# Performance work log

Measured on AMD Instinct MI355X. Metric: run time of the kernel, lower is better.

Reference implementation:

```python
import jax, jax.numpy as jnp
import numpy as np

M, B, S, D, H = 8, 4, 512, 512, 8
HD = D // H  # head_dim = 64


def setup_inputs() -> dict:
    key = jax.random.key(0)
    k1, k2, k3 = jax.random.split(key, 3)
    x = jax.random.normal(k1, (M, B, S, D), dtype=jnp.float32)
    qkv_weight = jax.random.normal(k2, (M, D, 3 * D), dtype=jnp.float32) * 0.02
    proj_weight = jax.random.normal(k3, (M, D, D), dtype=jnp.float32) * 0.02
    return {"x": x, "qkv_weight": qkv_weight, "proj_weight": proj_weight}


def reference(x, qkv_weight, proj_weight):
    m, b, s, d = x.shape
    # model-axis batched QKV projection
    qkv = jnp.einsum('mbti,mio->mbto', x, qkv_weight)
    q, k, v = jnp.split(qkv, 3, axis=-1)
    # [m, b, h, s, hd]
    q = q.reshape(m, b, s, H, HD).transpose(0, 1, 3, 2, 4)
    k = k.reshape(m, b, s, H, HD).transpose(0, 1, 3, 2, 4)
    v = v.reshape(m, b, s, H, HD).transpose(0, 1, 3, 2, 4)
    att = jnp.einsum('mbhqd,mbhkd->mbhqk', q, k) / jnp.sqrt(jnp.float32(HD))
    causal = jnp.tril(jnp.ones((s, s), dtype=bool))
    att = jnp.where(causal, att, jnp.float32(-jnp.inf))
    att = jax.nn.softmax(att, axis=-1)
    y = jnp.einsum('mbhqk,mbhkd->mbhqd', att, v)
    y = y.transpose(0, 1, 3, 2, 4).reshape(m, b, s, d)
    return jnp.einsum('mbti,mio->mbto', y, proj_weight)
```

## Files before the change

### kernel.cpp

```cpp
#include <hip/hip_runtime.h>
#include <hip/hip_bf16.h>


typedef unsigned short u16;
typedef unsigned int u32;
typedef __attribute__((ext_vector_type(8))) short short8;
typedef __attribute__((ext_vector_type(4))) float f32x4;
typedef __attribute__((ext_vector_type(4))) unsigned short u16x4;
typedef __attribute__((ext_vector_type(8))) unsigned short u16x8;
typedef __attribute__((ext_vector_type(2))) unsigned int u32x2;

#define MFMA16(a, b, c) __builtin_amdgcn_mfma_f32_16x16x32_bf16((a), (b), (c), 0, 0, 0)

__device__ __forceinline__ u16 f2bf(float f) {
  union { __hip_bfloat16 h; u16 u; } cv;
  cv.h = __float2bfloat16(f);
  return cv.u;
}

__device__ __forceinline__ void gl_lds16(const u16* g, u16* l) {
  __builtin_amdgcn_global_load_lds(
      (const __attribute__((address_space(1))) void*)g,
      (__attribute__((address_space(3))) void*)l, 16, 0, 0);
}

__global__ __launch_bounds__(256) void xcast_kernel(const float* __restrict__ in,
                                                    u16* __restrict__ out, long n8) {
  long stride = (long)gridDim.x * 256;
  for (long i = blockIdx.x * 256L + threadIdx.x; i < n8; i += stride) {
    f32x4 a = *(const f32x4*)(in + i * 8);
    f32x4 b = *(const f32x4*)(in + i * 8 + 4);
    u16x8 o = {f2bf(a[0]), f2bf(a[1]), f2bf(a[2]), f2bf(a[3]),
               f2bf(b[0]), f2bf(b[1]), f2bf(b[2]), f2bf(b[3])};
    *(u16x8*)(out + i * 8) = o;
  }
}

__global__ __launch_bounds__(256) void wtrans_kernel(const float* __restrict__ in,
                                                     u16* __restrict__ out, int R, int C) {
  __shared__ float t[32][33];
  int m = blockIdx.z;
  const float* pin = in + (size_t)m * R * C;
  u16* pout = out + (size_t)m * R * C;
  int c0 = blockIdx.x * 32, r0 = blockIdx.y * 32;
  int tx = threadIdx.x, ty = threadIdx.y;
#pragma unroll
  for (int i = 0; i < 4; ++i) {
    int r = ty + i * 8;
    t[r][tx] = pin[(size_t)(r0 + r) * C + c0 + tx];
  }
  __syncthreads();
#pragma unroll
  for (int i = 0; i < 4; ++i) {
    int r = ty + i * 8;
    pout[(size_t)(c0 + r) * R + r0 + tx] = f2bf(t[tx][r]);
  }
}

__global__ __launch_bounds__(512) void qkv_gemm_kernel(const u16* __restrict__ XB,
                                                       const u16* __restrict__ WT,
                                                       u16* __restrict__ Q,
                                                       u16* __restrict__ K,
                                                       u16* __restrict__ VT) {
  __shared__ __attribute__((aligned(16))) u16 As[3][256 * 32];
  __shared__ __attribute__((aligned(16))) u16 Bs[3][128 * 32];
  int bid = blockIdx.x;
  int wgid = (bid & 7) * 96 + (bid >> 3);
  int m = wgid / 96;
  int rem = wgid % 96;
  int r0 = (rem / 12) * 256, c0 = (rem % 12) * 128;
  const u16* A = XB + (size_t)m * 2048 * 512;
  const u16* BT = WT + (size_t)m * 1536 * 512;
  int t = threadIdx.x;
  int lane = t & 63, w = t >> 6;
  int wr = (w >> 1) * 64, wc = (w & 1) * 64;
  int fr = lane & 15, fc = lane >> 4;

  int rA0 = t >> 2, sA0 = (t & 3) ^ ((rA0 >> 1) & 3);
  int rA1 = 128 + (t >> 2), sA1 = (t & 3) ^ ((rA1 >> 1) & 3);

  f32x4 acc[4][4];
#pragma unroll
  for (int i = 0; i < 4; ++i)
#pragma unroll
    for (int j = 0; j < 4; ++j) acc[i][j] = f32x4{0.f, 0.f, 0.f, 0.f};

#define QKV_STAGE(tile)                                                            \
  {                                                                                \
    int kk_ = (tile) * 32;                                                         \
    int b_ = (tile) % 3;                                                           \
    gl_lds16(A + (size_t)(r0 + rA0) * 512 + kk_ + sA0 * 8, &As[b_][w * 512]);      \
    gl_lds16(A + (size_t)(r0 + rA1) * 512 + kk_ + sA1 * 8, &As[b_][4096 + w * 512]); \
    gl_lds16(BT + (size_t)(c0 + rA0) * 512 + kk_ + sA0 * 8, &Bs[b_][w * 512]);     \
  }

#define QKV_COMPUTE(tile)                                                          \
  {                                                                                \
    int b_ = (tile) % 3;                                                           \
    short8 af[4], bf_[4];                                                          \
    _Pragma("unroll") for (int i = 0; i < 4; ++i) {                                \
      int row = wr + i * 16 + fr;                                                  \
      int sl = fc ^ ((row >> 1) & 3);                                              \
      af[i] = *(const short8*)&As[b_][row * 32 + sl * 8];                          \
    }                                                                              \
    _Pragma("unroll") for (int j = 0; j < 4; ++j) {                                \
      int row = wc + j * 16 + fr;                                                  \
      int sl = fc ^ ((row >> 1) & 3);                                              \
      bf_[j] = *(const short8*)&Bs[b_][row * 32 + sl * 8];                         \
    }                                                                              \
    _Pragma("unroll") for (int i = 0; i < 4; ++i)                                  \
      _Pragma("unroll") for (int j = 0; j < 4; ++j)                                \
        acc[i][j] = MFMA16(af[i], bf_[j], acc[i][j]);                              \
  }

  QKV_STAGE(0);
  QKV_STAGE(1);
  for (int ks = 0; ks < 14; ++ks) {
    asm volatile("s_waitcnt vmcnt(3)" ::: "memory");
    __builtin_amdgcn_sched_barrier(0);
    __builtin_amdgcn_s_barrier();
    QKV_STAGE(ks + 2);
    QKV_COMPUTE(ks);
    __builtin_amdgcn_sched_barrier(0);
  }
  asm volatile("s_waitcnt vmcnt(0)" ::: "memory");
  __builtin_amdgcn_sched_barrier(0);
  __builtin_amdgcn_s_barrier();
  QKV_COMPUTE(14);
  QKV_COMPUTE(15);

  int seg = c0 >> 9;
  if (seg == 2) {
#pragma unroll
    for (int i = 0; i < 4; ++i)
#pragma unroll
      for (int j = 0; j < 4; ++j) {
        int s0 = r0 + wr + i * 16 + fc * 4;
        int gcol = c0 + wc + j * 16 + fr;
        int cc = gcol & 511;
        int hh = cc >> 6, hd = cc & 63;
        int b = s0 >> 9, s = s0 & 511;
        size_t headoff = (size_t)((m * 4 + b) * 8 + hh) * 32768;
        u16x4 pk = {f2bf(acc[i][j][0]), f2bf(acc[i][j][1]),
                    f2bf(acc[i][j][2]), f2bf(acc[i][j][3])};
        *(u16x4*)(VT + headoff + (size_t)hd * 512 + s) = pk;
      }
  } else {
#pragma unroll
    for (int i = 0; i < 4; ++i)
#pragma unroll
      for (int j = 0; j < 4; ++j)
#pragma unroll
        for (int r = 0; r < 4; ++r) {
          int grow = r0 + wr + i * 16 + fc * 4 + r;
          int gcol = c0 + wc + j * 16 + fr;
          int b = grow >> 9, s = grow & 511;
          int cc = gcol & 511;
          int hh = cc >> 6, hd = cc & 63;
          size_t headoff = (size_t)((m * 4 + b) * 8 + hh) * 32768;
          u16 val = f2bf(acc[i][j][r]);
          if (seg == 0) Q[headoff + s * 64 + hd] = val;
          else          K[headoff + s * 64 + hd] = val;
        }
  }
}

__global__ __launch_bounds__(256) void attn_kernel(const u16* __restrict__ Qg,
                                                   const u16* __restrict__ Kg,
                                                   const u16* __restrict__ VTg,
                                                   u16* __restrict__ Yg) {
  __shared__ __attribute__((aligned(16))) u16 Ks[2][64 * 64];
  __shared__ __attribute__((aligned(16))) u16 Vs[2][64 * 64];
  __shared__ u16 Pl[4][16][72];
  int bid = blockIdx.x;
  int p = bid >> 8;
  int g = bid & 255;
  int h = g & 7, mb = g >> 3;
  int qtA = p, qtB = 7 - p;
  int t = threadIdx.x, lane = t & 63, w = t >> 6;
  int fr = lane & 15, fc = lane >> 4;
  size_t hoff = ((size_t)mb * 8 + h) * 32768;
  const u16* Q = Qg + hoff;
  const u16* K = Kg + hoff;
  const u16* V = VTg + hoff;
  const float SC = 0.125f * 1.44269504088896340736f;

  int qrowA = qtA * 64 + w * 16 + fr;
  int qrowB = qtB * 64 + w * 16 + fr;
  short8 qA0 = *(const short8*)(Q + (size_t)qrowA * 64 + fc * 8);
  short8 qA1 = *(const short8*)(Q + (size_t)qrowA * 64 + 32 + fc * 8);
  short8 qB0 = *(const short8*)(Q + (size_t)qrowB * 64 + fc * 8);
  short8 qB1 = *(const short8*)(Q + (size_t)qrowB * 64 + 32 + fc * 8);

  f32x4 accA[4], accB[4];
#pragma unroll
  for (int d = 0; d < 4; ++d) {
    accA[d] = f32x4{0.f, 0.f, 0.f, 0.f};
    accB[d] = f32x4{0.f, 0.f, 0.f, 0.f};
  }
  float mstA = -1e30f, lstA = 0.f, mstB = -1e30f, lstB = 0.f;

  int sr0 = t >> 3, ss0 = (t & 7) ^ (sr0 & 7);
  int sr1 = 32 + (t >> 3), ss1 = (t & 7) ^ (sr1 & 7);

#define ATTN_STAGE(kt_, buf_)                                                     \
  {                                                                               \
    int kb_ = (kt_) * 64;                                                         \
    gl_lds16(K + (size_t)(kb_ + sr0) * 64 + ss0 * 8, &Ks[buf_][w * 512]);         \
    gl_lds16(K + (size_t)(kb_ + sr1) * 64 + ss1 * 8, &Ks[buf_][2048 + w * 512]);  \
    gl_lds16(V + (size_t)sr0 * 512 + kb_ + ss0 * 8, &Vs[buf_][w * 512]);          \
    gl_lds16(V + (size_t)sr1 * 512 + kb_ + ss1 * 8, &Vs[buf_][2048 + w * 512]);   \
  }

  int qloc = w * 16 + fr;
  ATTN_STAGE(0, 0);

  for (int kt = 0; kt <= qtB; ++kt) {
    int cur = kt & 1;
    if (kt < qtB) {
      ATTN_STAGE(kt + 1, cur ^ 1);
      asm volatile("s_waitcnt vmcnt(4)" ::: "memory");
    } else {
      asm volatile("s_waitcnt vmcnt(0)" ::: "memory");
    }
    __builtin_amdgcn_sched_barrier(0);
    __builtin_amdgcn_s_barrier();

    auto tile_compute = [&](const short8& qf0, const short8& qf1, f32x4(&acc)[4],
                            float& mst, float& lst, bool diag) {
      f32x4 st[4];
#pragma unroll
      for (int sub = 0; sub < 4; ++sub) {
        int row = sub * 16 + fr;
        short8 kf0 = *(const short8*)&Ks[cur][row * 64 + ((fc ^ (row & 7)) & 7) * 8];
        short8 kf1 = *(const short8*)&Ks[cur][row * 64 + (((4 + fc) ^ (row & 7)) & 7) * 8];
        f32x4 z = f32x4{0.f, 0.f, 0.f, 0.f};
        z = MFMA16(kf0, qf0, z);
        st[sub] = MFMA16(kf1, qf1, z);
      }
      float pv[4][4];
      float mt = -3e30f;
#pragma unroll
      for (int sub = 0; sub < 4; ++sub)
#pragma unroll
        for (int r = 0; r < 4; ++r) {
          float v = st[sub][r] * SC;
          if (diag && (sub * 16 + fc * 4 + r) > qloc) v = -1e30f;
          pv[sub][r] = v;
          mt = fmaxf(mt, v);
        }
      mt = fmaxf(mt, __shfl_xor(mt, 16));
      mt = fmaxf(mt, __shfl_xor(mt, 32));
      float mn = fmaxf(mst, mt);
      float al = __builtin_amdgcn_exp2f(mst - mn);
      mst = mn;
      float rs = 0.f;
#pragma unroll
      for (int sub = 0; sub < 4; ++sub)
#pragma unroll
        for (int r = 0; r < 4; ++r) {
          float e = __builtin_amdgcn_exp2f(pv[sub][r] - mn);
          pv[sub][r] = e;
          rs += e;
        }
      rs += __shfl_xor(rs, 16);
      rs += __shfl_xor(rs, 32);
      lst = lst * al + rs;
#pragma unroll
      for (int d = 0; d < 4; ++d) acc[d] *= al;

#pragma unroll
      for (int sub = 0; sub < 4; ++sub) {
        u32 lo = (u32)f2bf(pv[sub][0]) | ((u32)f2bf(pv[sub][1]) << 16);
        u32 hi = (u32)f2bf(pv[sub][2]) | ((u32)f2bf(pv[sub][3]) << 16);
        *(u32x2*)&Pl[w][fr][sub * 16 + fc * 4] = u32x2{lo, hi};
      }
#pragma unroll
      for (int dt = 0; dt < 4; ++dt)
#pragma unroll
        for (int kc = 0; kc < 2; ++kc) {
          int row = dt * 16 + fr;
          short8 vf = *(const short8*)&Vs[cur][row * 64 + (((kc * 4 + fc) ^ (row & 7)) & 7) * 8];
          short8 pb = *(const short8*)&Pl[w][fr][kc * 32 + fc * 8];
          acc[dt] = MFMA16(vf, pb, acc[dt]);
        }
    };

    if (kt <= qtA) tile_compute(qA0, qA1, accA, mstA, lstA, kt == qtA);
    tile_compute(qB0, qB1, accB, mstB, lstB, kt == qtB);

    asm volatile("s_waitcnt lgkmcnt(0)" ::: "memory");
    __builtin_amdgcn_sched_barrier(0);
    __builtin_amdgcn_s_barrier();
  }

  float invA = 1.0f / lstA, invB = 1.0f / lstB;
#pragma unroll
  for (int dt = 0; dt < 4; ++dt) {
    u16x4 oA = {f2bf(accA[dt][0] * invA), f2bf(accA[dt][1] * invA),
                f2bf(accA[dt][2] * invA), f2bf(accA[dt][3] * invA)};
    *(u16x4*)(Yg + ((size_t)mb * 512 + qrowA) * 512 + h * 64 + dt * 16 + fc * 4) = oA;
    u16x4 oB = {f2bf(accB[dt][0] * invB), f2bf(accB[dt][1] * invB),
                f2bf(accB[dt][2] * invB), f2bf(accB[dt][3] * invB)};
    *(u16x4*)(Yg + ((size_t)mb * 512 + qrowB) * 512 + h * 64 + dt * 16 + fc * 4) = oB;
  }
}

__global__ __launch_bounds__(512) void proj_gemm_kernel(const u16* __restrict__ Y,
                                                        const u16* __restrict__ PT,
                                                        float* __restrict__ OUT) {
  __shared__ __attribute__((aligned(16))) u16 As[3][256 * 32];
  __shared__ __attribute__((aligned(16))) u16 Bs[3][128 * 32];
  int bid = blockIdx.x;
  int wgid = (bid & 7) * 32 + (bid >> 3);
  int m = wgid / 32;
  int rem = wgid % 32;
  int r0 = (rem / 4) * 256, c0 = (rem % 4) * 128;
  const u16* A = Y + (size_t)m * 2048 * 512;
  const u16* BT = PT + (size_t)m * 512 * 512;
  float* C = OUT + (size_t)m * 2048 * 512;
  int t = threadIdx.x;
  int lane = t & 63, w = t >> 6;
  int wr = (w >> 1) * 64, wc = (w & 1) * 64;
  int fr = lane & 15, fc = lane >> 4;

  int rA0 = t >> 2, sA0 = (t & 3) ^ ((rA0 >> 1) & 3);
  int rA1 = 128 + (t >> 2), sA1 = (t & 3) ^ ((rA1 >> 1) & 3);

  f32x4 acc[4][4];
#pragma unroll
  for (int i = 0; i < 4; ++i)
#pragma unroll
    for (int j = 0; j < 4; ++j) acc[i][j] = f32x4{0.f, 0.f, 0.f, 0.f};

#define PROJ_STAGE(tile)                                                           \
  {                                                                                \
    int kk_ = (tile) * 32;                                                         \
    int b_ = (tile) % 3;                                                           \
    gl_lds16(A + (size_t)(r0 + rA0) * 512 + kk_ + sA0 * 8, &As[b_][w * 512]);      \
    gl_lds16(A + (size_t)(r0 + rA1) * 512 + kk_ + sA1 * 8, &As[b_][4096 + w * 512]); \
    gl_lds16(BT + (size_t)(c0 + rA0) * 512 + kk_ + sA0 * 8, &Bs[b_][w * 512]);     \
  }

#define PROJ_COMPUTE(tile)                                                         \
  {                                                                                \
    int b_ = (tile) % 3;                                                           \
    short8 af[4], bf_[4];                                                          \
    _Pragma("unroll") for (int i = 0; i < 4; ++i) {                                \
      int row = wr + i * 16 + fr;                                                  \
      int sl = fc ^ ((row >> 1) & 3);                                              \
      af[i] = *(const short8*)&As[b_][row * 32 + sl * 8];                          \
    }                                                                              \
    _Pragma("unroll") for (int j = 0; j < 4; ++j) {                                \
      int row = wc + j * 16 + fr;                                                  \
      int sl = fc ^ ((row >> 1) & 3);                                              \
      bf_[j] = *(const short8*)&Bs[b_][row * 32 + sl * 8];                         \
    }                                                                              \
    _Pragma("unroll") for (int i = 0; i < 4; ++i)                                  \
      _Pragma("unroll") for (int j = 0; j < 4; ++j)                                \
        acc[i][j] = MFMA16(af[i], bf_[j], acc[i][j]);                              \
  }

  PROJ_STAGE(0);
  PROJ_STAGE(1);
  for (int ks = 0; ks < 14; ++ks) {
    asm volatile("s_waitcnt vmcnt(3)" ::: "memory");
    __builtin_amdgcn_sched_barrier(0);
    __builtin_amdgcn_s_barrier();
    PROJ_STAGE(ks + 2);
    PROJ_COMPUTE(ks);
    __builtin_amdgcn_sched_barrier(0);
  }
  asm volatile("s_waitcnt vmcnt(0)" ::: "memory");
  __builtin_amdgcn_sched_barrier(0);
  __builtin_amdgcn_s_barrier();
  PROJ_COMPUTE(14);
  PROJ_COMPUTE(15);

#pragma unroll
  for (int i = 0; i < 4; ++i)
#pragma unroll
    for (int j = 0; j < 4; ++j)
#pragma unroll
      for (int r = 0; r < 4; ++r) {
        int grow = r0 + wr + i * 16 + fc * 4 + r;
        int gcol = c0 + wc + j * 16 + fr;
        C[(size_t)grow * 512 + gcol] = acc[i][j][r];
      }
}

extern "C" void kernel_launch(void* const* d_in, const int* in_sizes, int n_in,
                              void* d_out, int out_size, void* d_ws, size_t ws_size,
                              hipStream_t stream) {
  const float* x = (const float*)d_in[0];
  const float* wqkv = (const float*)d_in[1];
  const float* wproj = (const float*)d_in[2];
  float* out = (float*)d_out;

  u16* p = (u16*)d_ws;
  u16* wqkvT = p;  p += (size_t)8 * 1536 * 512;
  u16* wprojT = p; p += (size_t)8 * 512 * 512;
  u16* qb = p;     p += (size_t)8388608;
  u16* kb = p;     p += (size_t)8388608;
  u16* vtb = p;    p += (size_t)8388608;
  u16* xyb = p;    p += (size_t)8388608;

  xcast_kernel<<<2048, 256, 0, stream>>>(x, xyb, (long)8 * 4 * 512 * 512 / 8);
  wtrans_kernel<<<dim3(48, 16, 8), dim3(32, 8), 0, stream>>>(wqkv, wqkvT, 512, 1536);
  wtrans_kernel<<<dim3(16, 16, 8), dim3(32, 8), 0, stream>>>(wproj, wprojT, 512, 512);
  qkv_gemm_kernel<<<768, 512, 0, stream>>>(xyb, wqkvT, qb, kb, vtb);
  attn_kernel<<<1024, 256, 0, stream>>>(qb, kb, vtb, xyb);
  proj_gemm_kernel<<<256, 512, 0, stream>>>(xyb, wprojT, out);
}
```

Before: 190.4 us.

## Merge prep kernels and triple-buffer attention K/V tiles with one barrier per step

Folds the x cast and both weight transposes into a single prep kernel launch, removing two kernel launches and their gaps. Attention now keeps three K/V LDS buffers, issues the prefetch two tiles ahead after the top barrier, and drops the trailing lgkmcnt wait and second barrier of each iteration. This aims to hide more global-load latency and cut synchronisation, at the cost of more LDS per block, which may reduce occupancy. The vmcnt(4) wait still has to match the number of outstanding stage loads under the new prefetch distance.

```diff
diff --git a/kernel.cpp b/kernel.cpp
--- a/kernel.cpp
+++ b/kernel.cpp
@@ -24,36 +24,55 @@
       (__attribute__((address_space(3))) void*)l, 16, 0, 0);
 }
 
-__global__ __launch_bounds__(256) void xcast_kernel(const float* __restrict__ in,
-                                                    u16* __restrict__ out, long n8) {
-  long stride = (long)gridDim.x * 256;
-  for (long i = blockIdx.x * 256L + threadIdx.x; i < n8; i += stride) {
-    f32x4 a = *(const f32x4*)(in + i * 8);
-    f32x4 b = *(const f32x4*)(in + i * 8 + 4);
-    u16x8 o = {f2bf(a[0]), f2bf(a[1]), f2bf(a[2]), f2bf(a[3]),
-               f2bf(b[0]), f2bf(b[1]), f2bf(b[2]), f2bf(b[3])};
-    *(u16x8*)(out + i * 8) = o;
-  }
-}
-
-__global__ __launch_bounds__(256) void wtrans_kernel(const float* __restrict__ in,
-                                                     u16* __restrict__ out, int R, int C) {
-  __shared__ float t[32][33];
-  int m = blockIdx.z;
-  const float* pin = in + (size_t)m * R * C;
-  u16* pout = out + (size_t)m * R * C;
-  int c0 = blockIdx.x * 32, r0 = blockIdx.y * 32;
-  int tx = threadIdx.x, ty = threadIdx.y;
+__global__ __launch_bounds__(256) void prep_kernel(const float* __restrict__ x,
+                                                   u16* __restrict__ xb,
+                                                   const float* __restrict__ wqkv,
+                                                   u16* __restrict__ wqkvT,
+                                                   const float* __restrict__ wproj,
+                                                   u16* __restrict__ wprojT) {
+  __shared__ float tsh[32][33];
+  int bid = blockIdx.x;
+  int t = threadIdx.x;
+  if (bid < 1024) {
+    const long n8 = (long)8 * 4 * 512 * 512 / 8;
+    for (long i = (long)bid * 256 + t; i < n8; i += 1024L * 256) {
+      f32x4 a = *(const f32x4*)(x + i * 8);
+      f32x4 b = *(const f32x4*)(x + i * 8 + 4);
+      u16x8 o = {f2bf(a[0]), f2bf(a[1]), f2bf(a[2]), f2bf(a[3]),
+                 f2bf(b[0]), f2bf(b[1]), f2bf(b[2]), f2bf(b[3])};
+      *(u16x8*)(xb + i * 8) = o;
+    }
+    return;
+  }
+  const float* pin;
+  u16* pout;
+  int R = 512, C, r0, c0;
+  if (bid < 7168) {
+    int id = bid - 1024;
+    int m = id / 768, rem = id % 768;
+    int ry = rem / 48, cx = rem % 48;
+    C = 1536; r0 = ry * 32; c0 = cx * 32;
+    pin = wqkv + (size_t)m * 512 * 1536;
+    pout = wqkvT + (size_t)m * 512 * 1536;
+  } else {
+    int id = bid - 7168;
+    int m = id / 256, rem = id % 256;
+    int ry = rem / 16, cx = rem % 16;
+    C = 512; r0 = ry * 32; c0 = cx * 32;
+    pin = wproj + (size_t)m * 512 * 512;
+    pout = wprojT + (size_t)m * 512 * 512;
+  }
+  int tx = t & 31, ty = t >> 5;
 #pragma unroll
   for (int i = 0; i < 4; ++i) {
     int r = ty + i * 8;
-    t[r][tx] = pin[(size_t)(r0 + r) * C + c0 + tx];
+    tsh[r][tx] = pin[(size_t)(r0 + r) * C + c0 + tx];
   }
   __syncthreads();
 #pragma unroll
   for (int i = 0; i < 4; ++i) {
     int r = ty + i * 8;
-    pout[(size_t)(c0 + r) * R + r0 + tx] = f2bf(t[tx][r]);
+    pout[(size_t)(c0 + r) * R + r0 + tx] = f2bf(tsh[tx][r]);
   }
 }
 
@@ -169,8 +188,8 @@
                                                    const u16* __restrict__ Kg,
                                                    const u16* __restrict__ VTg,
                                                    u16* __restrict__ Yg) {
-  __shared__ __attribute__((aligned(16))) u16 Ks[2][64 * 64];
-  __shared__ __attribute__((aligned(16))) u16 Vs[2][64 * 64];
+  __shared__ __attribute__((aligned(16))) u16 Ks[3][64 * 64];
+  __shared__ __attribute__((aligned(16))) u16 Vs[3][64 * 64];
   __shared__ u16 Pl[4][16][72];
   int bid = blockIdx.x;
   int p = bid >> 8;
@@ -214,17 +233,21 @@
 
   int qloc = w * 16 + fr;
   ATTN_STAGE(0, 0);
+  ATTN_STAGE(1, 1);
+  int cur = 0;
 
   for (int kt = 0; kt <= qtB; ++kt) {
-    int cur = kt & 1;
     if (kt < qtB) {
-      ATTN_STAGE(kt + 1, cur ^ 1);
       asm volatile("s_waitcnt vmcnt(4)" ::: "memory");
     } else {
       asm volatile("s_waitcnt vmcnt(0)" ::: "memory");
     }
     __builtin_amdgcn_sched_barrier(0);
     __builtin_amdgcn_s_barrier();
+    if (kt + 2 <= qtB) {
+      int nb = (cur >= 1) ? cur - 1 : 2;
+      ATTN_STAGE(kt + 2, nb);
+    }
 
     auto tile_compute = [&](const short8& qf0, const short8& qf1, f32x4(&acc)[4],
                             float& mst, float& lst, bool diag) {
@@ -289,9 +312,8 @@
     if (kt <= qtA) tile_compute(qA0, qA1, accA, mstA, lstA, kt == qtA);
     tile_compute(qB0, qB1, accB, mstB, lstB, kt == qtB);
 
-    asm volatile("s_waitcnt lgkmcnt(0)" ::: "memory");
-    __builtin_amdgcn_sched_barrier(0);
-    __builtin_amdgcn_s_barrier();
+    __builtin_amdgcn_sched_barrier(0);
+    cur = (cur == 2) ? 0 : cur + 1;
   }
 
   float invA = 1.0f / lstA, invB = 1.0f / lstB;
@@ -405,9 +427,7 @@
   u16* vtb = p;    p += (size_t)8388608;
   u16* xyb = p;    p += (size_t)8388608;
 
-  xcast_kernel<<<2048, 256, 0, stream>>>(x, xyb, (long)8 * 4 * 512 * 512 / 8);
-  wtrans_kernel<<<dim3(48, 16, 8), dim3(32, 8), 0, stream>>>(wqkv, wqkvT, 512, 1536);
-  wtrans_kernel<<<dim3(16, 16, 8), dim3(32, 8), 0, stream>>>(wproj, wprojT, 512, 512);
+  prep_kernel<<<9216, 256, 0, stream>>>(x, xyb, wqkv, wqkvT, wproj, wprojT);
   qkv_gemm_kernel<<<768, 512, 0, stream>>>(xyb, wqkvT, qb, kb, vtb);
   attn_kernel<<<1024, 256, 0, stream>>>(qb, kb, vtb, xyb);
   proj_gemm_kernel<<<256, 512, 0, stream>>>(xyb, wprojT, out);
```

After: 188.0 us. About the same (-1.3%).
